# Kernel tuning notes

Measured on AMD Instinct MI355X. Metric: run time of the kernel, lower is better.

The kernel has to match this reference:

```python
import jax, jax.numpy as jnp
import numpy as np

N = 100000
E = 1600000
D = 128
H = 64
C = 10
G = 1024  # number of graphs in the batch


def setup_inputs() -> dict:
    key = jax.random.key(0)
    ks = jax.random.split(key, 12)
    x = jax.random.normal(ks[0], (N, D), dtype=jnp.float32)
    edge_index = jax.random.randint(ks[1], (2, E), 0, N, dtype=jnp.int64)
    batch = jnp.sort(jax.random.randint(ks[2], (N,), 0, G, dtype=jnp.int64))
    def glorot(k, fan_in, fan_out):
        s = jnp.sqrt(6.0 / (fan_in + fan_out))
        return jax.random.uniform(k, (fan_in, fan_out), jnp.float32, -s, s)
    W1 = glorot(ks[3], D, H); b1 = jnp.zeros((H,), jnp.float32)
    W2 = glorot(ks[4], H, H); b2 = jnp.zeros((H,), jnp.float32)
    W3 = glorot(ks[5], H, H); b3 = jnp.zeros((H,), jnp.float32)
    Wl = glorot(ks[6], H, C); bl = jnp.zeros((C,), jnp.float32)
    return {"x": x, "edge_index": edge_index, "batch": batch,
            "W1": W1, "b1": b1, "W2": W2, "b2": b2,
            "W3": W3, "b3": b3, "Wl": Wl, "bl": bl}


def gcn_conv(x, row, col, dinv, W, b):
    # PyG GCNConv: x' = D^-1/2 (A + I) D^-1/2 (x W) + b
    xw = x @ W                                   # (N, H)
    norm = dinv[row] * dinv[col]                 # (E+N,)
    msg = xw[row] * norm[:, None]                # gather + scale
    out = jax.ops.segment_sum(msg, col, num_segments=N)
    return out + b


def reference(x, edge_index, batch, W1, b1, W2, b2, W3, b3, Wl, bl):
    # add self loops once; normalization coefficients shared by all layers
    loop = jnp.arange(N, dtype=edge_index.dtype)
    row = jnp.concatenate([edge_index[0], loop])
    col = jnp.concatenate([edge_index[1], loop])
    deg = jax.ops.segment_sum(jnp.ones_like(col, dtype=x.dtype), col, num_segments=N)
    dinv = jnp.where(deg > 0, jax.lax.rsqrt(deg), 0.0)

    h = gcn_conv(x, row, col, dinv, W1, b1)
    h = gcn_conv(h, row, col, dinv, W2, b2)
    h = gcn_conv(h, row, col, dinv, W3, b3)

    # global mean pool over graphs
    sums = jax.ops.segment_sum(h, batch, num_segments=G)          # (G, H)
    cnts = jax.ops.segment_sum(jnp.ones((N,), h.dtype), batch, num_segments=G)
    pooled = sums / jnp.maximum(cnts, 1.0)[:, None]

    # dropout(p=0.5) is identity in eval mode
    return pooled @ Wl + bl                                        # (G, C)
```

## Files before the change

kernel.cpp:

```cpp
#include <hip/hip_runtime.h>

#define NN 100000
#define EE 1600000
#define DI 128
#define HH 64
#define CO 10
#define PADF 16
#define GG 1024
#define BSH 7
#define BNODES (1 << BSH)
#define NB ((NN + BNODES - 1) / BNODES)
#define TILE 4096
#define NT ((EE + TILE - 1) / TILE)
#define SN (NB * NT)
#define SCB 1024
#define NSB ((SN + SCB - 1) / SCB)
#define LPN 4

__global__ __launch_bounds__(256) void k_front(const int* __restrict__ col,
                                               const float* __restrict__ W1, const float* __restrict__ W2,
                                               const float* __restrict__ W3, const float* __restrict__ Wl,
                                               const float* __restrict__ b1, const float* __restrict__ b2,
                                               const float* __restrict__ b3,
                                               const int* __restrict__ batch,
                                               int* __restrict__ cnt, float* __restrict__ Wf,
                                               float* __restrict__ cvec, int* __restrict__ gstart) {
    __shared__ float smem[1280];
    int bid = blockIdx.x, t = threadIdx.x;
    if (bid < NT) {
        int* h = (int*)smem;
        for (int i = t; i < NB; i += 256) h[i] = 0;
        __syncthreads();
        int base = bid * TILE, end = min(base + TILE, EE);
        for (int e = base + t; e < end; e += 256)
            atomicAdd(&h[__builtin_nontemporal_load(&col[e]) >> BSH], 1);
        __syncthreads();
        for (int i = t; i < NB; i += 256) cnt[i * NT + bid] = h[i];
    } else if (bid == NT) {
        float* M3l = smem;
        float* M23l = smem + 640;
        for (int i = t; i < HH * CO; i += 256) {
            int r = i / CO, c = i % CO;
            float s = 0.f;
            for (int k = 0; k < HH; ++k) s += W3[r * HH + k] * Wl[k * CO + c];
            M3l[i] = s;
        }
        __syncthreads();
        for (int i = t; i < HH * CO; i += 256) {
            int r = i / CO, c = i % CO;
            float s = 0.f;
            for (int k = 0; k < HH; ++k) s += W2[r * HH + k] * M3l[k * CO + c];
            M23l[i] = s;
        }
        __syncthreads();
        for (int i = t; i < DI * CO; i += 256) {
            int r = i / CO, c = i % CO;
            float s = 0.f;
            for (int k = 0; k < HH; ++k) s += W1[r * HH + k] * M23l[k * CO + c];
            Wf[i] = s;
        }
        if (t < CO) {
            float s1 = 0.f, s2 = 0.f, s3 = 0.f;
            for (int k = 0; k < HH; ++k) {
                s1 += b1[k] * M23l[k * CO + t];
                s2 += b2[k] * M3l[k * CO + t];
                s3 += b3[k] * Wl[k * CO + t];
            }
            cvec[t] = s1; cvec[CO + t] = s2; cvec[2 * CO + t] = s3;
        }
    } else {
        int g = (bid - NT - 1) * 256 + t;
        if (g <= GG) {
            int lo = 0, hi = NN;
            while (lo < hi) { int mid = (lo + hi) >> 1; if (batch[mid] < g) lo = mid + 1; else hi = mid; }
            gstart[g] = lo;
        }
    }
}

__global__ __launch_bounds__(SCB) void k_scanA(int* __restrict__ a, int* __restrict__ bsum) {
    __shared__ int s[SCB];
    int t = threadIdx.x, idx = blockIdx.x * SCB + t;
    int v = (idx < SN) ? a[idx] : 0;
    s[t] = v;
    __syncthreads();
    for (int off = 1; off < SCB; off <<= 1) {
        int u = (t >= off) ? s[t - off] : 0;
        __syncthreads();
        s[t] += u;
        __syncthreads();
    }
    if (idx < SN) a[idx] = s[t] - v;
    if (t == SCB - 1) bsum[blockIdx.x] = s[t];
}
__global__ __launch_bounds__(SCB) void k_scanC(int* __restrict__ a, const int* __restrict__ bsum) {
    __shared__ int red[SCB];
    int t = threadIdx.x, bid = blockIdx.x;
    int partial = 0;
    for (int i = t; i < bid; i += SCB) partial += bsum[i];
    red[t] = partial;
    __syncthreads();
    for (int off = SCB / 2; off > 0; off >>= 1) {
        if (t < off) red[t] += red[t + off];
        __syncthreads();
    }
    int idx = bid * SCB + t;
    if (idx < SN) a[idx] += red[0];
}

__global__ __launch_bounds__(256) void k_pscatter(const int* __restrict__ row, const int* __restrict__ col,
                                                  const int* __restrict__ S, unsigned* __restrict__ ebuf) {
    __shared__ int ofs[NB];
    for (int i = threadIdx.x; i < NB; i += 256) ofs[i] = S[i * NT + blockIdx.x];
    __syncthreads();
    int base = blockIdx.x * TILE;
    int end = min(base + TILE, EE);
    for (int e = base + threadIdx.x; e < end; e += 256) {
        int c = __builtin_nontemporal_load(&col[e]);
        int r = __builtin_nontemporal_load(&row[e]);
        int pos = atomicAdd(&ofs[c >> BSH], 1);
        ebuf[pos] = ((unsigned)r << BSH) | (unsigned)(c & (BNODES - 1));
    }
}

__global__ __launch_bounds__(256) void k_bsort(const unsigned* __restrict__ ebuf, const int* __restrict__ S,
                                               int* __restrict__ srcIdx, int* __restrict__ rowptr_end,
                                               float* __restrict__ dinv) {
    __shared__ int cnt[BNODES];
    __shared__ int s[BNODES];
    __shared__ int ofs[BNODES];
    int t = threadIdx.x;
    int b = blockIdx.x;
    if (t < BNODES) cnt[t] = 0;
    __syncthreads();
    int beg = S[b * NT];
    int end = (b + 1 < NB) ? S[(b + 1) * NT] : EE;
    for (int e = beg + t; e < end; e += 256)
        atomicAdd(&cnt[__builtin_nontemporal_load(&ebuf[e]) & (BNODES - 1)], 1);
    __syncthreads();
    int v = 0;
    if (t < BNODES) { v = cnt[t]; s[t] = v; }
    __syncthreads();
    for (int off = 1; off < BNODES; off <<= 1) {
        int u = 0;
        if (t < BNODES && t >= off) u = s[t - off];
        __syncthreads();
        if (t < BNODES) s[t] += u;
        __syncthreads();
    }
    if (t < BNODES) {
        int n = (b << BSH) + t;
        if (n < NN) {
            dinv[n] = rsqrtf((float)(v + 1));
            rowptr_end[n] = beg + s[t];
        }
        ofs[t] = beg + s[t] - v;
    }
    __syncthreads();
    for (int e = beg + t; e < end; e += 256) {
        unsigned p = __builtin_nontemporal_load(&ebuf[e]);
        int pos = atomicAdd(&ofs[p & (BNODES - 1)], 1);
        srcIdx[pos] = (int)(p >> BSH);
    }
}

__global__ __launch_bounds__(256) void k_xw(const float* __restrict__ x, const float* __restrict__ Wf,
                                            const float* __restrict__ dinv,
                                            float* __restrict__ as_) {
    __shared__ float sWf[DI * CO];
    for (int i = threadIdx.x; i < DI * CO; i += blockDim.x) sWf[i] = Wf[i];
    __syncthreads();
    int gid = blockIdx.x * 256 + threadIdx.x;
    if (gid >= NN) return;
    int p = gid >> 1, c0 = (gid & 1) * 5;
    int n0 = 2 * p, n1 = n0 + 1;
    float a0[5] = {0, 0, 0, 0, 0}, a1[5] = {0, 0, 0, 0, 0};
    const float4* x0 = (const float4*)(x + (size_t)n0 * DI);
    const float4* x1 = (const float4*)(x + (size_t)n1 * DI);
#pragma unroll 4
    for (int d4 = 0; d4 < DI / 4; ++d4) {
        float4 u = x0[d4], v = x1[d4];
        const float* w = &sWf[d4 * 4 * CO + c0];
#pragma unroll
        for (int c = 0; c < 5; ++c) {
            float w0 = w[c], w1 = w[CO + c], w2 = w[2 * CO + c], w3 = w[3 * CO + c];
            a0[c] += u.x * w0 + u.y * w1 + u.z * w2 + u.w * w3;
            a1[c] += v.x * w0 + v.y * w1 + v.z * w2 + v.w * w3;
        }
    }
    float d0 = dinv[n0], d1 = dinv[n1];
    float* r0 = as_ + (size_t)n0 * PADF + c0;
    float* r1 = as_ + (size_t)n1 * PADF + c0;
#pragma unroll
    for (int c = 0; c < 5; ++c) {
        r0[c] = a0[c] * d0;
        r1[c] = a1[c] * d1;
    }
}

template <int FINAL>
__global__ __launch_bounds__(256) void k_gather(const int* __restrict__ rowptr_end,
                                                const int* __restrict__ srcIdx,
                                                const float* __restrict__ src,
                                                const float* __restrict__ dinv,
                                                const float* __restrict__ cvec, int coff,
                                                float* __restrict__ dst) {
    int gid = blockIdx.x * 256 + threadIdx.x;
    int n = gid >> 2;
    int l = threadIdx.x & (LPN - 1);
    if (n >= NN) return;
    int beg = (n == 0) ? 0 : rowptr_end[n - 1];
    int end = rowptr_end[n];
    float acc[CO];
#pragma unroll
    for (int c = 0; c < CO; ++c) acc[c] = 0.f;
    for (int e = beg + l; e < end; e += LPN) {
        int s = __builtin_nontemporal_load(&srcIdx[e]);
        const float* sp = src + (size_t)s * PADF;
        float4 a = ((const float4*)sp)[0];
        float4 b = ((const float4*)sp)[1];
        float2 c2 = ((const float2*)(sp + 8))[0];
        acc[0] += a.x; acc[1] += a.y; acc[2] += a.z; acc[3] += a.w;
        acc[4] += b.x; acc[5] += b.y; acc[6] += b.z; acc[7] += b.w;
        acc[8] += c2.x; acc[9] += c2.y;
    }
#pragma unroll
    for (int m = 1; m < LPN; m <<= 1) {
#pragma unroll
        for (int c = 0; c < CO; ++c) acc[c] += __shfl_xor(acc[c], m, 64);
    }
    if (l == 0) {
        float di = dinv[n];
        const float* selfp = src + (size_t)n * PADF;
        float o[CO];
#pragma unroll
        for (int c = 0; c < CO; ++c) {
            float y = di * (acc[c] + selfp[c]) + cvec[coff + c];
            o[c] = FINAL ? y : y * di;
        }
        float* dp = dst + (size_t)n * PADF;
        ((float4*)dp)[0] = make_float4(o[0], o[1], o[2], o[3]);
        ((float4*)dp)[1] = make_float4(o[4], o[5], o[6], o[7]);
        ((float2*)(dp + 8))[0] = make_float2(o[8], o[9]);
    }
}

__global__ __launch_bounds__(64) void k_pool(const float* __restrict__ h,
                                             const int* __restrict__ gstart,
                                             const float* __restrict__ bl,
                                             float* __restrict__ out) {
    int g = blockIdx.x;
    int beg = gstart[g], end = gstart[g + 1];
    int l = threadIdx.x;
    float acc[CO];
#pragma unroll
    for (int c = 0; c < CO; ++c) acc[c] = 0.f;
    for (int n = beg + l; n < end; n += 64) {
        const float* sp = h + (size_t)n * PADF;
        float4 a = ((const float4*)sp)[0];
        float4 b = ((const float4*)sp)[1];
        float2 c2 = ((const float2*)(sp + 8))[0];
        acc[0] += a.x; acc[1] += a.y; acc[2] += a.z; acc[3] += a.w;
        acc[4] += b.x; acc[5] += b.y; acc[6] += b.z; acc[7] += b.w;
        acc[8] += c2.x; acc[9] += c2.y;
    }
#pragma unroll
    for (int m = 1; m < 64; m <<= 1) {
#pragma unroll
        for (int c = 0; c < CO; ++c) acc[c] += __shfl_xor(acc[c], m, 64);
    }
    if (l == 0) {
        float cf = fmaxf((float)(end - beg), 1.f);
#pragma unroll
        for (int c = 0; c < CO; ++c) out[(size_t)g * CO + c] = acc[c] / cf + bl[c];
    }
}

extern "C" void kernel_launch(void* const* d_in, const int* in_sizes, int n_in,
                              void* d_out, int out_size, void* d_ws, size_t ws_size,
                              hipStream_t stream) {
    const float* x    = (const float*)d_in[0];
    const int*   ei   = (const int*)d_in[1];
    const int*   batch= (const int*)d_in[2];
    const float* W1   = (const float*)d_in[3];
    const float* b1   = (const float*)d_in[4];
    const float* W2   = (const float*)d_in[5];
    const float* b2   = (const float*)d_in[6];
    const float* W3   = (const float*)d_in[7];
    const float* b3   = (const float*)d_in[8];
    const float* Wl   = (const float*)d_in[9];
    const float* bl   = (const float*)d_in[10];
    float* out = (float*)d_out;

    const int* row = ei;
    const int* col = ei + EE;

    float* ws = (float*)d_ws;
    size_t off = 0;
    auto alloc = [&](size_t elems) { size_t cur = off; off += (elems + 63) & ~(size_t)63; return cur; };
    float*    Wf      = ws + alloc(DI * CO);
    float*    cvec    = ws + alloc(3 * CO);
    float*    dinv    = ws + alloc(NN);
    int*      S       = (int*)(ws + alloc(SN));
    int*      bsum    = (int*)(ws + alloc(NSB + 64));
    unsigned* ebuf    = (unsigned*)(ws + alloc(EE));
    int*      srcIdx  = (int*)(ws + alloc(EE));
    int*      rowptr  = (int*)(ws + alloc(NN));
    float*    as_     = ws + alloc((size_t)NN * PADF);
    float*    bbuf    = ws + alloc((size_t)NN * PADF);
    int*      gstart  = (int*)(ws + alloc(GG + 1));
    (void)ws_size; (void)in_sizes; (void)n_in; (void)out_size;

    const int BT = 256;
    int gN = (NN + BT - 1) / BT;
    int gNL = ((NN * LPN) + BT - 1) / BT;
    int gFront = NT + 1 + (GG + 1 + BT - 1) / BT;

    hipLaunchKernelGGL(k_front,    dim3(gFront), dim3(256), 0, stream,
                       col, W1, W2, W3, Wl, b1, b2, b3, batch, S, Wf, cvec, gstart);
    hipLaunchKernelGGL(k_scanA,    dim3(NSB), dim3(SCB), 0, stream, S, bsum);
    hipLaunchKernelGGL(k_scanC,    dim3(NSB), dim3(SCB), 0, stream, S, bsum);
    hipLaunchKernelGGL(k_pscatter, dim3(NT),  dim3(256), 0, stream, row, col, S, ebuf);
    hipLaunchKernelGGL(k_bsort,    dim3(NB),  dim3(256), 0, stream, ebuf, S, srcIdx, rowptr, dinv);
    hipLaunchKernelGGL(k_xw,       dim3(gN),  dim3(BT), 0, stream, x, Wf, dinv, as_);

    hipLaunchKernelGGL((k_gather<0>), dim3(gNL), dim3(BT), 0, stream, rowptr, srcIdx, as_,  dinv, cvec, 0,      bbuf);
    hipLaunchKernelGGL((k_gather<0>), dim3(gNL), dim3(BT), 0, stream, rowptr, srcIdx, bbuf, dinv, cvec, CO,     as_);
    hipLaunchKernelGGL((k_gather<1>), dim3(gNL), dim3(BT), 0, stream, rowptr, srcIdx, as_,  dinv, cvec, 2 * CO, bbuf);

    hipLaunchKernelGGL(k_pool, dim3(GG), dim3(64), 0, stream, bbuf, gstart, bl, out);
}
```

Measured before the change: 277.8 us.

## Fuse edge scatter with x·Wf projection and defer dinv scaling to first gather

```diff
diff --git a/kernel.cpp b/kernel.cpp
--- a/kernel.cpp
+++ b/kernel.cpp
@@ -8,7 +8,7 @@
 #define PADF 16
 #define GG 1024
 #define BSH 7
-#define BNODES (1 << BSH)
+#define BNODES 128
 #define NB ((NN + BNODES - 1) / BNODES)
 #define TILE 4096
 #define NT ((EE + TILE - 1) / TILE)
@@ -16,6 +16,7 @@
 #define SCB 1024
 #define NSB ((SN + SCB - 1) / SCB)
 #define LPN 4
+#define BT 256
 
 __global__ __launch_bounds__(256) void k_front(const int* __restrict__ col,
                                                const float* __restrict__ W1, const float* __restrict__ W2,
@@ -40,22 +41,19 @@
         float* M3l = smem;
         float* M23l = smem + 640;
         for (int i = t; i < HH * CO; i += 256) {
-            int r = i / CO, c = i % CO;
-            float s = 0.f;
+            int r = i / CO, c = i % CO; float s = 0.f;
             for (int k = 0; k < HH; ++k) s += W3[r * HH + k] * Wl[k * CO + c];
             M3l[i] = s;
         }
         __syncthreads();
         for (int i = t; i < HH * CO; i += 256) {
-            int r = i / CO, c = i % CO;
-            float s = 0.f;
+            int r = i / CO, c = i % CO; float s = 0.f;
             for (int k = 0; k < HH; ++k) s += W2[r * HH + k] * M3l[k * CO + c];
             M23l[i] = s;
         }
         __syncthreads();
         for (int i = t; i < DI * CO; i += 256) {
-            int r = i / CO, c = i % CO;
-            float s = 0.f;
+            int r = i / CO, c = i % CO; float s = 0.f;
             for (int k = 0; k < HH; ++k) s += W1[r * HH + k] * M23l[k * CO + c];
             Wf[i] = s;
         }
@@ -108,18 +106,48 @@
     if (idx < SN) a[idx] += red[0];
 }
 
-__global__ __launch_bounds__(256) void k_pscatter(const int* __restrict__ row, const int* __restrict__ col,
-                                                  const int* __restrict__ S, unsigned* __restrict__ ebuf) {
-    __shared__ int ofs[NB];
-    for (int i = threadIdx.x; i < NB; i += 256) ofs[i] = S[i * NT + blockIdx.x];
-    __syncthreads();
-    int base = blockIdx.x * TILE;
-    int end = min(base + TILE, EE);
-    for (int e = base + threadIdx.x; e < end; e += 256) {
-        int c = __builtin_nontemporal_load(&col[e]);
-        int r = __builtin_nontemporal_load(&row[e]);
-        int pos = atomicAdd(&ofs[c >> BSH], 1);
-        ebuf[pos] = ((unsigned)r << BSH) | (unsigned)(c & (BNODES - 1));
+__global__ __launch_bounds__(256) void k_sxw(const int* __restrict__ row, const int* __restrict__ col,
+                                             const int* __restrict__ S, unsigned* __restrict__ ebuf,
+                                             const float* __restrict__ x, const float* __restrict__ Wf,
+                                             float* __restrict__ as_) {
+    __shared__ float smf[DI * CO];
+    int* smi = (int*)smf;
+    int bid = blockIdx.x, t = threadIdx.x;
+    if (bid < NT) {
+        for (int i = t; i < NB; i += 256) smi[i] = S[i * NT + bid];
+        __syncthreads();
+        int base = bid * TILE, end = min(base + TILE, EE);
+        for (int e = base + t; e < end; e += 256) {
+            int c = __builtin_nontemporal_load(&col[e]);
+            int r = __builtin_nontemporal_load(&row[e]);
+            int pos = atomicAdd(&smi[c >> BSH], 1);
+            ebuf[pos] = ((unsigned)r << BSH) | (unsigned)(c & (BNODES - 1));
+        }
+    } else {
+        for (int i = t; i < DI * CO; i += 256) smf[i] = Wf[i];
+        __syncthreads();
+        int gid = (bid - NT) * 256 + t;
+        if (gid >= NN) return;
+        int pr = gid >> 1, c0 = (gid & 1) * 5;
+        int n0 = 2 * pr, n1 = n0 + 1;
+        float a0[5] = {0, 0, 0, 0, 0}, a1[5] = {0, 0, 0, 0, 0};
+        const float4* x0 = (const float4*)(x + (size_t)n0 * DI);
+        const float4* x1 = (const float4*)(x + (size_t)n1 * DI);
+#pragma unroll 4
+        for (int d4 = 0; d4 < DI / 4; ++d4) {
+            float4 u = x0[d4], v = x1[d4];
+            const float* w = &smf[d4 * 4 * CO + c0];
+#pragma unroll
+            for (int c = 0; c < 5; ++c) {
+                float w0 = w[c], w1 = w[CO + c], w2 = w[2 * CO + c], w3 = w[3 * CO + c];
+                a0[c] += u.x * w0 + u.y * w1 + u.z * w2 + u.w * w3;
+                a1[c] += v.x * w0 + v.y * w1 + v.z * w2 + v.w * w3;
+            }
+        }
+        float* r0 = as_ + (size_t)n0 * PADF + c0;
+        float* r1 = as_ + (size_t)n1 * PADF + c0;
+#pragma unroll
+        for (int c = 0; c < 5; ++c) { r0[c] = a0[c]; r1[c] = a1[c]; }
     }
 }
 
@@ -164,41 +192,7 @@
     }
 }
 
-__global__ __launch_bounds__(256) void k_xw(const float* __restrict__ x, const float* __restrict__ Wf,
-                                            const float* __restrict__ dinv,
-                                            float* __restrict__ as_) {
-    __shared__ float sWf[DI * CO];
-    for (int i = threadIdx.x; i < DI * CO; i += blockDim.x) sWf[i] = Wf[i];
-    __syncthreads();
-    int gid = blockIdx.x * 256 + threadIdx.x;
-    if (gid >= NN) return;
-    int p = gid >> 1, c0 = (gid & 1) * 5;
-    int n0 = 2 * p, n1 = n0 + 1;
-    float a0[5] = {0, 0, 0, 0, 0}, a1[5] = {0, 0, 0, 0, 0};
-    const float4* x0 = (const float4*)(x + (size_t)n0 * DI);
-    const float4* x1 = (const float4*)(x + (size_t)n1 * DI);
-#pragma unroll 4
-    for (int d4 = 0; d4 < DI / 4; ++d4) {
-        float4 u = x0[d4], v = x1[d4];
-        const float* w = &sWf[d4 * 4 * CO + c0];
-#pragma unroll
-        for (int c = 0; c < 5; ++c) {
-            float w0 = w[c], w1 = w[CO + c], w2 = w[2 * CO + c], w3 = w[3 * CO + c];
-            a0[c] += u.x * w0 + u.y * w1 + u.z * w2 + u.w * w3;
-            a1[c] += v.x * w0 + v.y * w1 + v.z * w2 + v.w * w3;
-        }
-    }
-    float d0 = dinv[n0], d1 = dinv[n1];
-    float* r0 = as_ + (size_t)n0 * PADF + c0;
-    float* r1 = as_ + (size_t)n1 * PADF + c0;
-#pragma unroll
-    for (int c = 0; c < 5; ++c) {
-        r0[c] = a0[c] * d0;
-        r1[c] = a1[c] * d1;
-    }
-}
-
-template <int FINAL>
+template <int MODE>
 __global__ __launch_bounds__(256) void k_gather(const int* __restrict__ rowptr_end,
                                                 const int* __restrict__ srcIdx,
                                                 const float* __restrict__ src,
@@ -220,9 +214,16 @@
         float4 a = ((const float4*)sp)[0];
         float4 b = ((const float4*)sp)[1];
         float2 c2 = ((const float2*)(sp + 8))[0];
-        acc[0] += a.x; acc[1] += a.y; acc[2] += a.z; acc[3] += a.w;
-        acc[4] += b.x; acc[5] += b.y; acc[6] += b.z; acc[7] += b.w;
-        acc[8] += c2.x; acc[9] += c2.y;
+        if (MODE == 0) {
+            float w = dinv[s];
+            acc[0] += w * a.x; acc[1] += w * a.y; acc[2] += w * a.z; acc[3] += w * a.w;
+            acc[4] += w * b.x; acc[5] += w * b.y; acc[6] += w * b.z; acc[7] += w * b.w;
+            acc[8] += w * c2.x; acc[9] += w * c2.y;
+        } else {
+            acc[0] += a.x; acc[1] += a.y; acc[2] += a.z; acc[3] += a.w;
+            acc[4] += b.x; acc[5] += b.y; acc[6] += b.z; acc[7] += b.w;
+            acc[8] += c2.x; acc[9] += c2.y;
+        }
     }
 #pragma unroll
     for (int m = 1; m < LPN; m <<= 1) {
@@ -232,11 +233,16 @@
     if (l == 0) {
         float di = dinv[n];
         const float* selfp = src + (size_t)n * PADF;
+        float4 sa = ((const float4*)selfp)[0];
+        float4 sb = ((const float4*)selfp)[1];
+        float2 sc = ((const float2*)(selfp + 8))[0];
+        float self[CO] = {sa.x, sa.y, sa.z, sa.w, sb.x, sb.y, sb.z, sb.w, sc.x, sc.y};
         float o[CO];
 #pragma unroll
         for (int c = 0; c < CO; ++c) {
-            float y = di * (acc[c] + selfp[c]) + cvec[coff + c];
-            o[c] = FINAL ? y : y * di;
+            float sv = (MODE == 0) ? di * self[c] : self[c];
+            float y = di * (acc[c] + sv) + cvec[coff + c];
+            o[c] = (MODE == 2) ? y : y * di;
         }
         float* dp = dst + (size_t)n * PADF;
         ((float4*)dp)[0] = make_float4(o[0], o[1], o[2], o[3]);
@@ -311,22 +317,20 @@
     int*      gstart  = (int*)(ws + alloc(GG + 1));
     (void)ws_size; (void)in_sizes; (void)n_in; (void)out_size;
 
-    const int BT = 256;
-    int gN = (NN + BT - 1) / BT;
     int gNL = ((NN * LPN) + BT - 1) / BT;
     int gFront = NT + 1 + (GG + 1 + BT - 1) / BT;
-
-    hipLaunchKernelGGL(k_front,    dim3(gFront), dim3(256), 0, stream,
+    int gSxw = NT + (NN + BT - 1) / BT;
+
+    hipLaunchKernelGGL(k_front,    dim3(gFront), dim3(BT), 0, stream,
                        col, W1, W2, W3, Wl, b1, b2, b3, batch, S, Wf, cvec, gstart);
     hipLaunchKernelGGL(k_scanA,    dim3(NSB), dim3(SCB), 0, stream, S, bsum);
     hipLaunchKernelGGL(k_scanC,    dim3(NSB), dim3(SCB), 0, stream, S, bsum);
-    hipLaunchKernelGGL(k_pscatter, dim3(NT),  dim3(256), 0, stream, row, col, S, ebuf);
-    hipLaunchKernelGGL(k_bsort,    dim3(NB),  dim3(256), 0, stream, ebuf, S, srcIdx, rowptr, dinv);
-    hipLaunchKernelGGL(k_xw,       dim3(gN),  dim3(BT), 0, stream, x, Wf, dinv, as_);
+    hipLaunchKernelGGL(k_sxw,      dim3(gSxw), dim3(BT), 0, stream, row, col, S, ebuf, x, Wf, as_);
+    hipLaunchKernelGGL(k_bsort,    dim3(NB),  dim3(BT), 0, stream, ebuf, S, srcIdx, rowptr, dinv);
 
     hipLaunchKernelGGL((k_gather<0>), dim3(gNL), dim3(BT), 0, stream, rowptr, srcIdx, as_,  dinv, cvec, 0,      bbuf);
-    hipLaunchKernelGGL((k_gather<0>), dim3(gNL), dim3(BT), 0, stream, rowptr, srcIdx, bbuf, dinv, cvec, CO,     as_);
-    hipLaunchKernelGGL((k_gather<1>), dim3(gNL), dim3(BT), 0, stream, rowptr, srcIdx, as_,  dinv, cvec, 2 * CO, bbuf);
+    hipLaunchKernelGGL((k_gather<1>), dim3(gNL), dim3(BT), 0, stream, rowptr, srcIdx, bbuf, dinv, cvec, CO,     as_);
+    hipLaunchKernelGGL((k_gather<2>), dim3(gNL), dim3(BT), 0, stream, rowptr, srcIdx, as_,  dinv, cvec, 2 * CO, bbuf);
 
     hipLaunchKernelGGL(k_pool, dim3(GG), dim3(64), 0, stream, bbuf, gstart, bl, out);
 }
```

Result: slower. 288.8 us (+3.9%).
